# Kernel optimization log

Measured on AMD Instinct MI355X. Metric: run time of the kernel, lower is better.

## Reference

```python
import jax, jax.numpy as jnp
import numpy as np

EPS = 1e-5
NHEAD = 8

def layer_norm(x, g, b):
    mu = jnp.mean(x, axis=-1, keepdims=True)
    var = jnp.mean((x - mu) ** 2, axis=-1, keepdims=True)
    return (x - mu) * jax.lax.rsqrt(var + EPS) * g + b

def setup_inputs() -> dict:
    key = jax.random.key(0)
    ks = jax.random.split(key, 8)
    B, S, D, F = 4, 2048, 512, 2048
    s = 0.02
    return {
        "x": jax.random.normal(ks[0], (B, S, D), jnp.float32),
        "Wqkv": jax.random.normal(ks[1], (3 * D, D), jnp.float32) * s,
        "bqkv": jnp.zeros((3 * D,), jnp.float32),
        "Wo": jax.random.normal(ks[2], (D, D), jnp.float32) * s,
        "bo": jnp.zeros((D,), jnp.float32),
        "W1": jax.random.normal(ks[3], (F, D), jnp.float32) * s,
        "b1": jnp.zeros((F,), jnp.float32),
        "W2": jax.random.normal(ks[4], (D, F), jnp.float32) * s,
        "b2": jnp.zeros((D,), jnp.float32),
        "g1": jnp.ones((D,), jnp.float32),
        "bn1": jnp.zeros((D,), jnp.float32),
        "g2": jnp.ones((D,), jnp.float32),
        "bn2": jnp.zeros((D,), jnp.float32),
    }

def reference(x, Wqkv, bqkv, Wo, bo, W1, b1, W2, b2, g1, bn1, g2, bn2):
    B, S, D = x.shape
    H = NHEAD
    hd = D // H
    # fused QKV projection (torch MultiheadAttention in_proj)
    qkv = x @ Wqkv.T + bqkv                      # [B,S,3D]
    q, k, v = jnp.split(qkv, 3, axis=-1)
    q = q.reshape(B, S, H, hd).transpose(0, 2, 1, 3)  # [B,H,S,hd]
    k = k.reshape(B, S, H, hd).transpose(0, 2, 1, 3)
    v = v.reshape(B, S, H, hd).transpose(0, 2, 1, 3)
    scores = jnp.einsum("bhqd,bhkd->bhqk", q, k) / jnp.sqrt(jnp.float32(hd))
    causal = jnp.tril(jnp.ones((S, S), bool))
    scores = jnp.where(causal, scores, jnp.float32(-jnp.inf))
    attn = jax.nn.softmax(scores, axis=-1)
    ctx = jnp.einsum("bhqk,bhkd->bhqd", attn, v)        # [B,H,S,hd]
    ctx = ctx.transpose(0, 2, 1, 3).reshape(B, S, D)
    attn_out = ctx @ Wo.T + bo
    # residual + LayerNorm 1
    x = layer_norm(x + attn_out, g1, bn1)
    # FFN (ReLU) + residual + LayerNorm 2
    ff = jax.nn.relu(x @ W1.T + b1) @ W2.T + b2
    x = layer_norm(x + ff, g2, bn2)
    return x
```

## Files before the change

kernel.cpp:

```cpp
#include <hip/hip_runtime.h>
#include <hip/hip_bf16.h>
#include <math.h>

#define D_MODEL 512
#define SEQ     2048
#define BATCH   4
#define NHEADS  8
#define HDIM    64
#define FFN     2048
#define TOKENS  (BATCH*SEQ)

typedef __attribute__((ext_vector_type(8))) short bf16x8;
typedef __attribute__((ext_vector_type(4))) float f32x4;
typedef __attribute__((ext_vector_type(4))) unsigned u32x4;

__device__ inline ushort f2bf(float f) {
    unsigned u = __builtin_bit_cast(unsigned, f);
    unsigned r = (u + 0x7fffu + ((u >> 16) & 1u)) >> 16;
    return (ushort)r;
}

#define GLOAD_LDS16(g, l) __builtin_amdgcn_global_load_lds( \
    (const __attribute__((address_space(1))) void*)(g), \
    (__attribute__((address_space(3))) void*)(l), 16, 0, 0)

__global__ void cast_all_bf16(const float* __restrict__ x, const float* __restrict__ Wqkv,
                              const float* __restrict__ Wo, const float* __restrict__ W1,
                              const float* __restrict__ W2, ushort* __restrict__ outbase) {
    const int i = blockIdx.x * blockDim.x + threadIdx.x;
    if (i >= 1835008) return;
    float4 v;
    if      (i < 1048576) v = ((const float4*)x)[i];
    else if (i < 1245184) v = ((const float4*)Wqkv)[i - 1048576];
    else if (i < 1310720) v = ((const float4*)Wo)[i - 1245184];
    else if (i < 1572864) v = ((const float4*)W1)[i - 1310720];
    else                  v = ((const float4*)W2)[i - 1572864];
    ushort4 o;
    o.x = f2bf(v.x); o.y = f2bf(v.y); o.z = f2bf(v.z); o.w = f2bf(v.w);
    ((ushort4*)outbase)[i] = o;
}

template<int MODE, int RELU>
__global__ __launch_bounds__(256) void gemm_bt_mfma(const ushort* __restrict__ A,
                                                    const ushort* __restrict__ W,
                                                    const float* __restrict__ bias,
                                                    void* __restrict__ CoutA,
                                                    void* __restrict__ CoutB,
                                                    ushort* __restrict__ Qc,
                                                    ushort* __restrict__ Kc,
                                                    ushort* __restrict__ Vt,
                                                    int M, int N, int Kstride, int Klen) {
    __shared__ ushort Asb[128 * 32];
    __shared__ ushort Bsb[128 * 32];

    const int tid  = threadIdx.x;
    const int lane = tid & 63;
    const int wv   = tid >> 6;
    const int m0   = blockIdx.y * 128;
    const int n0   = blockIdx.x * 128;
    const int wm   = (wv >> 1) * 64;
    const int wn   = (wv & 1) * 64;
    const int ksel = (MODE == 3) ? blockIdx.z : 0;

    const ushort* Ab = A + (size_t)ksel * Klen;
    const ushort* Wb = W + (size_t)ksel * Klen;

    const int eA = wv * 1024 + lane * 8;
    const int rA = eA >> 5, cA = eA & 31;
    const ushort* gA0 = Ab + (size_t)(m0 + rA) * Kstride + cA;
    const ushort* gA1 = gA0 + (size_t)16 * Kstride;
    const ushort* gB0 = Wb + (size_t)(n0 + rA) * Kstride + cA;
    const ushort* gB1 = gB0 + (size_t)16 * Kstride;
    ushort* lA0 = Asb + wv * 1024;
    ushort* lA1 = Asb + wv * 1024 + 512;
    ushort* lB0 = Bsb + wv * 1024;
    ushort* lB1 = Bsb + wv * 1024 + 512;

    f32x4 acc[4][4] = {};

    const int fr = lane & 15;
    const int fk = (lane >> 4) * 8;

    for (int k0 = 0; k0 < Klen; k0 += 32) {
        GLOAD_LDS16(gA0, lA0); GLOAD_LDS16(gA1, lA1);
        GLOAD_LDS16(gB0, lB0); GLOAD_LDS16(gB1, lB1);
        gA0 += 32; gA1 += 32; gB0 += 32; gB1 += 32;
        __syncthreads();

        bf16x8 af[4], bfr[4];
        #pragma unroll
        for (int i = 0; i < 4; ++i)
            af[i] = *(const bf16x8*)(Asb + (wm + i * 16 + fr) * 32 + fk);
        #pragma unroll
        for (int j = 0; j < 4; ++j)
            bfr[j] = *(const bf16x8*)(Bsb + (wn + j * 16 + fr) * 32 + fk);

        #pragma unroll
        for (int i = 0; i < 4; ++i)
            #pragma unroll
            for (int j = 0; j < 4; ++j)
                acc[i][j] = __builtin_amdgcn_mfma_f32_16x16x32_bf16(af[i], bfr[j], acc[i][j], 0, 0, 0);
        __syncthreads();
    }

    const int col  = lane & 15;
    const int rowq = (lane >> 4) * 4;
    #pragma unroll
    for (int i = 0; i < 4; ++i) {
        const int gm = m0 + wm + i * 16 + rowq;
        #pragma unroll
        for (int j = 0; j < 4; ++j) {
            const int gn = n0 + wn + j * 16 + col;
            if (MODE == 2) {
                const float bv = bias[gn];
                const int seg = gn >> 9;
                const int h   = (gn >> 6) & 7;
                const int dd  = gn & 63;
                const int bb  = gm >> 11;
                const int ss  = gm & 2047;
                const int bh  = bb * 8 + h;
                if (seg == 2) {
                    ushort4 pk;
                    pk.x = f2bf(acc[i][j][0] + bv);
                    pk.y = f2bf(acc[i][j][1] + bv);
                    pk.z = f2bf(acc[i][j][2] + bv);
                    pk.w = f2bf(acc[i][j][3] + bv);
                    *(ushort4*)(Vt + ((size_t)bh * 64 + dd) * 2048 + ss) = pk;
                } else {
                    ushort* dst = (seg == 0 ? Qc : Kc) + ((size_t)bh * 2048 + ss) * 64 + dd;
                    #pragma unroll
                    for (int r = 0; r < 4; ++r)
                        dst[(size_t)r * 64] = f2bf(acc[i][j][r] + bv);
                }
            } else if (MODE == 3) {
                float* dst = (float*)(ksel ? CoutB : CoutA);
                const float bv = ksel ? 0.f : bias[gn];
                #pragma unroll
                for (int r = 0; r < 4; ++r)
                    dst[(size_t)(gm + r) * N + gn] = acc[i][j][r] + bv;
            } else {
                const float bv = bias[gn];
                #pragma unroll
                for (int r = 0; r < 4; ++r) {
                    float v = acc[i][j][r] + bv;
                    if (RELU) v = fmaxf(v, 0.f);
                    ((ushort*)CoutA)[(size_t)(gm + r) * N + gn] = f2bf(v);
                }
            }
        }
    }
}

__device__ __forceinline__ void attn_step(const ushort* __restrict__ Kb,
                                          const ushort* __restrict__ Vb,
                                          bf16x8 qf0, bf16x8 qf1,
                                          float& lp, f32x4 (&o)[4],
                                          int qw, int j0, bool diag,
                                          int col, int g, int c7) {
    f32x4 s[4] = {};
    #pragma unroll
    for (int nt = 0; nt < 4; ++nt) {
        const int kr = nt * 16 + col;
        bf16x8 kf0 = *(const bf16x8*)(Kb + kr * 64 + (((g    ) ^ c7) * 8));
        bf16x8 kf1 = *(const bf16x8*)(Kb + kr * 64 + (((g + 4) ^ c7) * 8));
        s[nt] = __builtin_amdgcn_mfma_f32_16x16x32_bf16(kf0, qf0, s[nt], 0, 0, 0);
        s[nt] = __builtin_amdgcn_mfma_f32_16x16x32_bf16(kf1, qf1, s[nt], 0, 0, 0);
    }

    if (diag) {
        #pragma unroll
        for (int nt = 0; nt < 4; ++nt)
            #pragma unroll
            for (int r = 0; r < 4; ++r)
                if ((j0 + nt * 16 + 4 * g + r) > (qw + col)) s[nt][r] = -INFINITY;
    }

    unsigned W[8];
    #pragma unroll
    for (int nt = 0; nt < 4; ++nt) {
        float p0 = __expf(s[nt][0] * 0.125f);
        float p1 = __expf(s[nt][1] * 0.125f);
        float p2 = __expf(s[nt][2] * 0.125f);
        float p3 = __expf(s[nt][3] * 0.125f);
        lp += (p0 + p1) + (p2 + p3);
        asm("v_cvt_pk_bf16_f32 %0, %1, %2" : "=v"(W[2 * nt])     : "v"(p0), "v"(p1));
        asm("v_cvt_pk_bf16_f32 %0, %1, %2" : "=v"(W[2 * nt + 1]) : "v"(p2), "v"(p3));
    }
    asm("v_permlane32_swap_b32 %0, %1" : "+v"(W[0]), "+v"(W[2]));
    asm("v_permlane32_swap_b32 %0, %1" : "+v"(W[1]), "+v"(W[3]));
    asm("v_permlane32_swap_b32 %0, %1" : "+v"(W[4]), "+v"(W[6]));
    asm("v_permlane32_swap_b32 %0, %1" : "+v"(W[5]), "+v"(W[7]));
    asm("v_permlane16_swap_b32 %0, %1" : "+v"(W[0]), "+v"(W[2]));
    asm("v_permlane16_swap_b32 %0, %1" : "+v"(W[1]), "+v"(W[3]));
    asm("v_permlane16_swap_b32 %0, %1" : "+v"(W[4]), "+v"(W[6]));
    asm("v_permlane16_swap_b32 %0, %1" : "+v"(W[5]), "+v"(W[7]));

    u32x4 wa = {W[0], W[1], W[2], W[3]};
    u32x4 wb = {W[4], W[5], W[6], W[7]};
    bf16x8 pf0 = __builtin_bit_cast(bf16x8, wa);
    bf16x8 pf1 = __builtin_bit_cast(bf16x8, wb);

    #pragma unroll
    for (int nt = 0; nt < 4; ++nt) {
        const int vr = nt * 16 + col;
        bf16x8 vf0 = *(const bf16x8*)(Vb + vr * 64 + (((g    ) ^ c7) * 8));
        bf16x8 vf1 = *(const bf16x8*)(Vb + vr * 64 + (((g + 4) ^ c7) * 8));
        o[nt] = __builtin_amdgcn_mfma_f32_16x16x32_bf16(pf0, vf0, o[nt], 0, 0, 0);
        o[nt] = __builtin_amdgcn_mfma_f32_16x16x32_bf16(pf1, vf1, o[nt], 0, 0, 0);
    }
}

__global__ __launch_bounds__(256, 4) void attn_mfma_kernel(const ushort* __restrict__ Qc,
                                                           const ushort* __restrict__ Kc,
                                                           const ushort* __restrict__ Vt,
                                                           ushort* __restrict__ ctxb) {
    __shared__ ushort Ks[2 * 64 * 64];
    __shared__ ushort Vs[2 * 64 * 64];

    const int tid  = threadIdx.x;
    const int lane = tid & 63;
    const int wv   = tid >> 6;
    const int idx  = blockIdx.x;
    const int bh   = (idx & 7) * 4 + (idx >> 7);
    const int pair = (idx >> 3) & 15;
    const int q0a  = pair * 64;
    const int q0b  = (31 - pair) * 64;
    const int qwA  = q0a + wv * 16;
    const int qwB  = q0b + wv * 16;

    const int col = lane & 15;
    const int g   = lane >> 4;
    const int c7  = col & 7;

    bf16x8 qfA0, qfA1, qfB0, qfB1;
    {
        const ushort* qa = Qc + ((size_t)bh * 2048 + qwA + col) * 64 + g * 8;
        qfA0 = *(const bf16x8*)qa;
        qfA1 = *(const bf16x8*)(qa + 32);
        const ushort* qb = Qc + ((size_t)bh * 2048 + qwB + col) * 64 + g * 8;
        qfB0 = *(const bf16x8*)qb;
        qfB1 = *(const bf16x8*)(qb + 32);
    }

    const int srow = tid >> 2;
    const int sch  = 2 * (tid & 3);
    const ushort* Kg = Kc + ((size_t)bh * 2048 + srow) * 64 + sch * 8;
    const ushort* Vg = Vt + ((size_t)bh * 64 + srow) * 2048 + sch * 8;
    const int ko0 = srow * 64 + (((sch    ) ^ (srow & 7)) * 8);
    const int ko1 = srow * 64 + (((sch + 1) ^ (srow & 7)) * 8);

    float lpa = 0.f, lpb = 0.f;
    f32x4 oa[4] = {}, ob[4] = {};

    bf16x8 pk0 = *(const bf16x8*)(Kg);
    bf16x8 pk1 = *(const bf16x8*)(Kg + 8);
    bf16x8 pv0 = *(const bf16x8*)(Vg);
    bf16x8 pv1 = *(const bf16x8*)(Vg + 8);

    for (int j0 = 0; j0 <= q0b; j0 += 64) {
        const int par = (j0 >> 6) & 1;
        ushort* Kb = Ks + par * 4096;
        ushort* Vb = Vs + par * 4096;
        *(bf16x8*)(Kb + ko0) = pk0; *(bf16x8*)(Kb + ko1) = pk1;
        *(bf16x8*)(Vb + ko0) = pv0; *(bf16x8*)(Vb + ko1) = pv1;
        __syncthreads();

        if (j0 < q0b) {
            pk0 = *(const bf16x8*)(Kg + (size_t)(j0 + 64) * 64);
            pk1 = *(const bf16x8*)(Kg + (size_t)(j0 + 64) * 64 + 8);
            pv0 = *(const bf16x8*)(Vg + j0 + 64);
            pv1 = *(const bf16x8*)(Vg + j0 + 72);
        }

        if (j0 <= q0a)
            attn_step(Kb, Vb, qfA0, qfA1, lpa, oa, qwA, j0, j0 == q0a, col, g, c7);
        attn_step(Kb, Vb, qfB0, qfB1, lpb, ob, qwB, j0, j0 == q0b, col, g, c7);
    }

    float la = lpa; la += __shfl_xor(la, 16); la += __shfl_xor(la, 32);
    float lb = lpb; lb += __shfl_xor(lb, 16); lb += __shfl_xor(lb, 32);
    const int b = bh >> 3, h = bh & 7;
    #pragma unroll
    for (int r = 0; r < 4; ++r) {
        const float inva = 1.f / __shfl(la, 4 * g + r);
        const float invb = 1.f / __shfl(lb, 4 * g + r);
        const size_t rowa = ((size_t)b * 2048 + qwA + 4 * g + r) * 512 + h * 64;
        const size_t rowb = ((size_t)b * 2048 + qwB + 4 * g + r) * 512 + h * 64;
        #pragma unroll
        for (int nt = 0; nt < 4; ++nt) {
            ctxb[rowa + nt * 16 + col] = f2bf(oa[nt][r] * inva);
            ctxb[rowb + nt * 16 + col] = f2bf(ob[nt][r] * invb);
        }
    }
}

template<int WRITE_BF16>
__global__ void ln_residual(const float* __restrict__ A, const float* __restrict__ B1,
                            const float* __restrict__ B2,
                            const float* __restrict__ g, const float* __restrict__ beta,
                            float* __restrict__ out, ushort* __restrict__ outb) {
    __shared__ float sbuf[8];
    const int row = blockIdx.x;
    const int tid = threadIdx.x;
    const size_t base = (size_t)row * D_MODEL;

    float v0 = A[base + tid]       + B1[base + tid]       + B2[base + tid];
    float v1 = A[base + tid + 256] + B1[base + tid + 256] + B2[base + tid + 256];

    float sum = v0 + v1;
    #pragma unroll
    for (int off = 32; off; off >>= 1) sum += __shfl_xor(sum, off);
    if ((tid & 63) == 0) sbuf[tid >> 6] = sum;
    __syncthreads();
    if (tid == 0) { float t = 0.f; for (int i = 0; i < 4; ++i) t += sbuf[i]; sbuf[4] = t; }
    __syncthreads();
    const float mu = sbuf[4] * (1.f / 512.f);
    __syncthreads();

    float d0 = v0 - mu, d1 = v1 - mu;
    float sq = d0 * d0 + d1 * d1;
    #pragma unroll
    for (int off = 32; off; off >>= 1) sq += __shfl_xor(sq, off);
    if ((tid & 63) == 0) sbuf[tid >> 6] = sq;
    __syncthreads();
    if (tid == 0) { float t = 0.f; for (int i = 0; i < 4; ++i) t += sbuf[i]; sbuf[4] = t; }
    __syncthreads();
    const float var = sbuf[4] * (1.f / 512.f);
    const float rs  = rsqrtf(var + 1e-5f);

    float r0 = d0 * rs * g[tid]       + beta[tid];
    float r1 = d1 * rs * g[tid + 256] + beta[tid + 256];
    out[base + tid]       = r0;
    out[base + tid + 256] = r1;
    if (WRITE_BF16) {
        outb[base + tid]       = f2bf(r0);
        outb[base + tid + 256] = f2bf(r1);
    }
}

extern "C" void kernel_launch(void* const* d_in, const int* in_sizes, int n_in,
                              void* d_out, int out_size, void* d_ws, size_t ws_size,
                              hipStream_t stream) {
    const float* x    = (const float*)d_in[0];
    const float* Wqkv = (const float*)d_in[1];
    const float* bqkv = (const float*)d_in[2];
    const float* Wo   = (const float*)d_in[3];
    const float* bo   = (const float*)d_in[4];
    const float* W1   = (const float*)d_in[5];
    const float* b1   = (const float*)d_in[6];
    const float* W2   = (const float*)d_in[7];
    const float* b2   = (const float*)d_in[8];
    const float* g1   = (const float*)d_in[9];
    const float* bn1  = (const float*)d_in[10];
    const float* g2   = (const float*)d_in[11];
    const float* bn2  = (const float*)d_in[12];

    float* ws = (float*)d_ws;
    ushort* Qcb     = (ushort*)ws;
    ushort* Kcb     = (ushort*)(ws + 2097152);
    ushort* Vtb     = (ushort*)(ws + 4194304);
    float*  attn_b  = ws;
    ushort* ff1b    = (ushort*)ws;
    float*  ff2a    = ws + 8388608;
    float*  attn_a  = ws + 12582912;
    float*  ff2b    = ws + 12582912;
    float*  ln1     = ws + 16777216;
    ushort* ctxb  = (ushort*)(ws + 20971520);
    ushort* ln1b  = (ushort*)(ws + 23068672);
    ushort* xb    = (ushort*)(ws + 25165824);
    ushort* Wqkvb = (ushort*)(ws + 27262976);
    float*  out   = (float*)d_out;
    ushort* W1b   = (ushort*)(ws + 27787264);
    ushort* W2b   = (ushort*)(ws + 28311552);
    ushort* Wob   = (ushort*)(ws + 27656192);

    const dim3 blk(256);

    cast_all_bf16<<<dim3(7168), blk, 0, stream>>>(x, Wqkv, Wo, W1, W2, xb);

    gemm_bt_mfma<2,0><<<dim3(1536/128, 8192/128), blk, 0, stream>>>(
        xb, Wqkvb, bqkv, nullptr, nullptr, Qcb, Kcb, Vtb, TOKENS, 1536, 512, 512);
    attn_mfma_kernel<<<dim3(512), blk, 0, stream>>>(Qcb, Kcb, Vtb, ctxb);
    gemm_bt_mfma<3,0><<<dim3(512/128, 8192/128, 2), blk, 0, stream>>>(
        ctxb, Wob, bo, attn_a, attn_b, nullptr, nullptr, nullptr, TOKENS, 512, 512, 256);
    ln_residual<1><<<dim3(TOKENS), blk, 0, stream>>>(x, attn_a, attn_b, g1, bn1, ln1, ln1b);
    gemm_bt_mfma<1,1><<<dim3(2048/128, 8192/128), blk, 0, stream>>>(
        ln1b, W1b, b1, ff1b, nullptr, nullptr, nullptr, nullptr, TOKENS, 2048, 512, 512);
    gemm_bt_mfma<3,0><<<dim3(512/128, 8192/128, 2), blk, 0, stream>>>(
        ff1b, W2b, b2, ff2a, ff2b, nullptr, nullptr, nullptr, TOKENS, 512, 2048, 1024);
    ln_residual<0><<<dim3(TOKENS), blk, 0, stream>>>(ln1, ff2a, ff2b, g2, bn2, out, nullptr);
}
```

Baseline: 265.0 us.

## Double-buffer GEMM LDS tiles and swizzle K-chunks to avoid bank conflicts

The bf16 MFMA GEMM now keeps two LDS buffers, so the global-to-LDS load of the next K tile is issued before the current tile is computed. This replaces the two barriers per iteration with a single waitcnt plus barrier. The column offset is also XOR-swizzled at the global source address and in the fragment reads, to reduce LDS bank conflicts. The cost is double the LDS per block, which may lower occupancy. The loop also assumes Klen is a multiple of 64.

```diff
diff --git a/kernel.cpp b/kernel.cpp
--- a/kernel.cpp
+++ b/kernel.cpp
@@ -50,8 +50,8 @@
                                                     ushort* __restrict__ Kc,
                                                     ushort* __restrict__ Vt,
                                                     int M, int N, int Kstride, int Klen) {
-    __shared__ ushort Asb[128 * 32];
-    __shared__ ushort Bsb[128 * 32];
+    __shared__ ushort Asb[2][128 * 32];
+    __shared__ ushort Bsb[2][128 * 32];
 
     const int tid  = threadIdx.x;
     const int lane = tid & 63;
@@ -65,43 +65,57 @@
     const ushort* Ab = A + (size_t)ksel * Klen;
     const ushort* Wb = W + (size_t)ksel * Klen;
 
-    const int eA = wv * 1024 + lane * 8;
-    const int rA = eA >> 5, cA = eA & 31;
-    const ushort* gA0 = Ab + (size_t)(m0 + rA) * Kstride + cA;
+    const int rA = wv * 32 + (lane >> 2);
+    const int cS = (((lane & 3) ^ ((lane >> 3) & 3)) * 8);
+    const ushort* gA0 = Ab + (size_t)(m0 + rA) * Kstride + cS;
     const ushort* gA1 = gA0 + (size_t)16 * Kstride;
-    const ushort* gB0 = Wb + (size_t)(n0 + rA) * Kstride + cA;
+    const ushort* gB0 = Wb + (size_t)(n0 + rA) * Kstride + cS;
     const ushort* gB1 = gB0 + (size_t)16 * Kstride;
-    ushort* lA0 = Asb + wv * 1024;
-    ushort* lA1 = Asb + wv * 1024 + 512;
-    ushort* lB0 = Bsb + wv * 1024;
-    ushort* lB1 = Bsb + wv * 1024 + 512;
 
     f32x4 acc[4][4] = {};
 
-    const int fr = lane & 15;
-    const int fk = (lane >> 4) * 8;
-
-    for (int k0 = 0; k0 < Klen; k0 += 32) {
-        GLOAD_LDS16(gA0, lA0); GLOAD_LDS16(gA1, lA1);
-        GLOAD_LDS16(gB0, lB0); GLOAD_LDS16(gB1, lB1);
-        gA0 += 32; gA1 += 32; gB0 += 32; gB1 += 32;
-        __syncthreads();
-
-        bf16x8 af[4], bfr[4];
-        #pragma unroll
-        for (int i = 0; i < 4; ++i)
-            af[i] = *(const bf16x8*)(Asb + (wm + i * 16 + fr) * 32 + fk);
-        #pragma unroll
-        for (int j = 0; j < 4; ++j)
-            bfr[j] = *(const bf16x8*)(Bsb + (wn + j * 16 + fr) * 32 + fk);
-
-        #pragma unroll
-        for (int i = 0; i < 4; ++i)
-            #pragma unroll
-            for (int j = 0; j < 4; ++j)
-                acc[i][j] = __builtin_amdgcn_mfma_f32_16x16x32_bf16(af[i], bfr[j], acc[i][j], 0, 0, 0);
-        __syncthreads();
-    }
+    const int fr  = lane & 15;
+    const int fks = (((lane >> 4) ^ ((fr >> 1) & 3)) * 8);
+
+#define STAGE(buf) do { \
+        GLOAD_LDS16(gA0, &Asb[buf][wv * 1024]); \
+        GLOAD_LDS16(gA1, &Asb[buf][wv * 1024 + 512]); \
+        GLOAD_LDS16(gB0, &Bsb[buf][wv * 1024]); \
+        GLOAD_LDS16(gB1, &Bsb[buf][wv * 1024 + 512]); \
+        gA0 += 32; gA1 += 32; gB0 += 32; gB1 += 32; } while (0)
+
+#define COMPUTE(buf) do { \
+        bf16x8 af_[4], bf_[4]; \
+        _Pragma("unroll") \
+        for (int i_ = 0; i_ < 4; ++i_) \
+            af_[i_] = *(const bf16x8*)(&Asb[buf][(wm + i_ * 16 + fr) * 32 + fks]); \
+        _Pragma("unroll") \
+        for (int j_ = 0; j_ < 4; ++j_) \
+            bf_[j_] = *(const bf16x8*)(&Bsb[buf][(wn + j_ * 16 + fr) * 32 + fks]); \
+        _Pragma("unroll") \
+        for (int i_ = 0; i_ < 4; ++i_) \
+            _Pragma("unroll") \
+            for (int j_ = 0; j_ < 4; ++j_) \
+                acc[i_][j_] = __builtin_amdgcn_mfma_f32_16x16x32_bf16(af_[i_], bf_[j_], acc[i_][j_], 0, 0, 0); \
+        } while (0)
+
+#define PSYNC do { \
+        asm volatile("s_waitcnt vmcnt(0)" ::: "memory"); \
+        __builtin_amdgcn_s_barrier(); \
+        __builtin_amdgcn_sched_barrier(0); } while (0)
+
+    STAGE(0);
+    PSYNC;
+    for (int it = (Klen >> 6) - 1; it > 0; --it) {
+        STAGE(1); COMPUTE(0); PSYNC;
+        STAGE(0); COMPUTE(1); PSYNC;
+    }
+    STAGE(1); COMPUTE(0); PSYNC;
+    COMPUTE(1);
+
+#undef STAGE
+#undef COMPUTE
+#undef PSYNC
 
     const int col  = lane & 15;
     const int rowq = (lane >> 4) * 4;
```

Result: no change. 268.8 us (+1.4%).
